# Performance work log

Measured on AMD Instinct MI355X. Metric: run time of the kernel, lower is better.

Reference implementation:

```python
import jax, jax.numpy as jnp
import numpy as np

B, S, D, E, K, FF = 4, 2048, 1024, 8, 2, 4096  # batch, seq, d_model, experts, top-k, 4*d_model


def setup_inputs() -> dict:
    key = jax.random.key(0)
    k0, k1, k2, k3 = jax.random.split(key, 4)
    scale = 0.02
    return {
        "x": jax.random.normal(k0, (B, S, D), jnp.float32),
        "gate_w": jax.random.normal(k1, (D, E), jnp.float32) * scale,
        "w1": jax.random.normal(k2, (E, D, FF), jnp.float32) * scale,
        "b1": jnp.zeros((E, FF), jnp.float32),
        "w2": jax.random.normal(k3, (E, FF, D), jnp.float32) * scale,
        "b2": jnp.zeros((E, D), jnp.float32),
    }


def reference(x, gate_w, w1, b1, w2, b2):
    # Gating: top-k logits, softmax over the selected k (matches torch.topk + softmax)
    logits = jnp.einsum("bsd,de->bse", x, gate_w)  # [B,S,E]
    vals, idxs = jax.lax.top_k(logits, K)           # [B,S,K]
    w = jax.nn.softmax(vals, axis=-1)               # [B,S,K]
    n_exp = gate_w.shape[-1]
    # Per-token combine weight for each expert (0 if not selected)
    combine = jnp.sum(jax.nn.one_hot(idxs, n_exp, dtype=x.dtype) * w[..., None], axis=-2)  # [B,S,E]

    out = jnp.zeros_like(x)
    for e in range(n_exp):  # fixed small loop over experts
        h = jax.nn.silu(jnp.einsum("bsd,df->bsf", x, w1[e]) + b1[e])  # dropout = identity (eval)
        y = jnp.einsum("bsf,fd->bsd", h, w2[e]) + b2[e]
        out = out + combine[..., e:e + 1] * y
    return out
```

## Files before the change

### kernel.cpp

```cpp
#include <hip/hip_runtime.h>
#include <math.h>

#define Tt 8192
#define Dd 1024
#define Ee 8
#define FFf 4096
#define SLOTS (Tt*2)

typedef unsigned short u16;
typedef unsigned int u32;
typedef __attribute__((ext_vector_type(8))) __bf16 bf16x8;
typedef __attribute__((ext_vector_type(4))) float f32x4;

__device__ __forceinline__ u16 f2bf(float f) {
  union { float f; u32 u; } v; v.f = f;
  u32 u = v.u;
  return (u16)((u + 0x7FFFu + ((u >> 16) & 1u)) >> 16);
}
__device__ __forceinline__ float bf2f(u16 h) {
  union { u32 u; float f; } v; v.u = ((u32)h) << 16; return v.f;
}
__device__ __forceinline__ void gl2lds16(const u16* g, u16* l) {
  __builtin_amdgcn_global_load_lds((const __attribute__((address_space(1))) void*)g,
                                   (__attribute__((address_space(3))) void*)l, 16, 0, 0);
}

__global__ void gate_topk_kernel(const float* __restrict__ x,
                                 const float* __restrict__ gw,
                                 int* __restrict__ counts,
                                 int* __restrict__ tok_e,
                                 float* __restrict__ tok_w) {
  int wave = (int)((blockIdx.x * blockDim.x + threadIdx.x) >> 6);
  int lane = threadIdx.x & 63;
  if (wave >= Tt) return;
  const float* xrow = x + (size_t)wave * Dd;
  float p[Ee];
#pragma unroll
  for (int e = 0; e < Ee; e++) p[e] = 0.f;
  int d0 = lane * 16;
#pragma unroll
  for (int i = 0; i < 16; i++) {
    float xv = xrow[d0 + i];
    const float* g = gw + (size_t)(d0 + i) * Ee;
#pragma unroll
    for (int e = 0; e < Ee; e++) p[e] += xv * g[e];
  }
#pragma unroll
  for (int e = 0; e < Ee; e++) {
    for (int off = 32; off > 0; off >>= 1) p[e] += __shfl_xor(p[e], off, 64);
  }
  if (lane == 0) {
    int e0 = 0; float v0 = p[0];
#pragma unroll
    for (int e = 1; e < Ee; e++) if (p[e] > v0) { v0 = p[e]; e0 = e; }
    int e1 = -1; float v1 = -INFINITY;
#pragma unroll
    for (int e = 0; e < Ee; e++) if (e != e0 && p[e] > v1) { v1 = p[e]; e1 = e; }
    float w0 = 1.f / (1.f + expf(v1 - v0));
    float w1 = 1.f - w0;
    tok_e[wave * 2 + 0] = e0; tok_e[wave * 2 + 1] = e1;
    tok_w[wave * 2 + 0] = w0; tok_w[wave * 2 + 1] = w1;
    atomicAdd(&counts[e0], 1);
    atomicAdd(&counts[e1], 1);
  }
}

__global__ void xb_convert_kernel(const float* __restrict__ x, u16* __restrict__ xb) {
  int i = blockIdx.x * blockDim.x + threadIdx.x;
  const float* s = x + (size_t)i * 8;
  f32x4 v0 = *(const f32x4*)(s);
  f32x4 v1 = *(const f32x4*)(s + 4);
  uint4 o;
  o.x = (u32)f2bf(v0[0]) | ((u32)f2bf(v0[1]) << 16);
  o.y = (u32)f2bf(v0[2]) | ((u32)f2bf(v0[3]) << 16);
  o.z = (u32)f2bf(v1[0]) | ((u32)f2bf(v1[1]) << 16);
  o.w = (u32)f2bf(v1[2]) | ((u32)f2bf(v1[3]) << 16);
  *(uint4*)(xb + (size_t)i * 8) = o;
}

__global__ __launch_bounds__(256) void wconv_kernel(const float* __restrict__ src,
                                                    u16* __restrict__ dst, int R, int C) {
  __shared__ u16 t[64][72];
  int e = blockIdx.z;
  size_t ebase = (size_t)e * R * C;
  int r0 = blockIdx.y * 64, c0 = blockIdx.x * 64;
  int tid = threadIdx.x;
  int row = tid >> 2, seg = tid & 3;
  const float* sp = src + ebase + (size_t)(r0 + row) * C + c0 + seg * 16;
  f32x4 v0 = *(const f32x4*)(sp);
  f32x4 v1 = *(const f32x4*)(sp + 4);
  f32x4 v2 = *(const f32x4*)(sp + 8);
  f32x4 v3 = *(const f32x4*)(sp + 12);
  uint4 o0, o1;
  o0.x = (u32)f2bf(v0[0]) | ((u32)f2bf(v0[1]) << 16);
  o0.y = (u32)f2bf(v0[2]) | ((u32)f2bf(v0[3]) << 16);
  o0.z = (u32)f2bf(v1[0]) | ((u32)f2bf(v1[1]) << 16);
  o0.w = (u32)f2bf(v1[2]) | ((u32)f2bf(v1[3]) << 16);
  o1.x = (u32)f2bf(v2[0]) | ((u32)f2bf(v2[1]) << 16);
  o1.y = (u32)f2bf(v2[2]) | ((u32)f2bf(v2[3]) << 16);
  o1.z = (u32)f2bf(v3[0]) | ((u32)f2bf(v3[1]) << 16);
  o1.w = (u32)f2bf(v3[2]) | ((u32)f2bf(v3[3]) << 16);
  *(uint4*)&t[row][seg * 16] = o0;
  *(uint4*)&t[row][seg * 16 + 8] = o1;
  __syncthreads();
  u32 w[8];
#pragma unroll
  for (int i = 0; i < 8; i++)
    w[i] = (u32)t[seg * 16 + 2 * i][row] | ((u32)t[seg * 16 + 2 * i + 1][row] << 16);
  u16* dp = dst + ebase + (size_t)(c0 + row) * R + r0 + seg * 16;
  uint4 d0, d1;
  d0.x = w[0]; d0.y = w[1]; d0.z = w[2]; d0.w = w[3];
  d1.x = w[4]; d1.y = w[5]; d1.z = w[6]; d1.w = w[7];
  *(uint4*)dp = d0;
  *(uint4*)(dp + 8) = d1;
}

__global__ void scan_kernel(const int* __restrict__ counts,
                            int* __restrict__ offsets, int* __restrict__ cursors) {
  if (threadIdx.x == 0 && blockIdx.x == 0) {
    int acc = 0;
    for (int e = 0; e < Ee; e++) { offsets[e] = acc; cursors[e] = acc; acc += counts[e]; }
  }
}

__global__ void scatter_kernel(const int* __restrict__ tok_e, const float* __restrict__ tok_w,
                               int* __restrict__ cursors,
                               int* __restrict__ slot_token, float* __restrict__ slot_w,
                               int* __restrict__ tok_slot) {
  int t = blockIdx.x * blockDim.x + threadIdx.x;
  if (t >= Tt) return;
#pragma unroll
  for (int k = 0; k < 2; k++) {
    int e = tok_e[t * 2 + k];
    int pos = atomicAdd(&cursors[e], 1);
    slot_token[pos] = t;
    slot_w[pos] = tok_w[t * 2 + k];
    tok_slot[t * 2 + k] = pos;
  }
}

#define MFMA16(H)                                                                 \
  do {                                                                            \
    acc[H][0][0] = __builtin_amdgcn_mfma_f32_16x16x32_bf16(a0, b0, acc[H][0][0], 0, 0, 0); \
    acc[H][0][1] = __builtin_amdgcn_mfma_f32_16x16x32_bf16(a0, b1, acc[H][0][1], 0, 0, 0); \
    acc[H][0][2] = __builtin_amdgcn_mfma_f32_16x16x32_bf16(a0, b2, acc[H][0][2], 0, 0, 0); \
    acc[H][0][3] = __builtin_amdgcn_mfma_f32_16x16x32_bf16(a0, b3, acc[H][0][3], 0, 0, 0); \
    acc[H][1][0] = __builtin_amdgcn_mfma_f32_16x16x32_bf16(a1, b0, acc[H][1][0], 0, 0, 0); \
    acc[H][1][1] = __builtin_amdgcn_mfma_f32_16x16x32_bf16(a1, b1, acc[H][1][1], 0, 0, 0); \
    acc[H][1][2] = __builtin_amdgcn_mfma_f32_16x16x32_bf16(a1, b2, acc[H][1][2], 0, 0, 0); \
    acc[H][1][3] = __builtin_amdgcn_mfma_f32_16x16x32_bf16(a1, b3, acc[H][1][3], 0, 0, 0); \
    acc[H][2][0] = __builtin_amdgcn_mfma_f32_16x16x32_bf16(a2, b0, acc[H][2][0], 0, 0, 0); \
    acc[H][2][1] = __builtin_amdgcn_mfma_f32_16x16x32_bf16(a2, b1, acc[H][2][1], 0, 0, 0); \
    acc[H][2][2] = __builtin_amdgcn_mfma_f32_16x16x32_bf16(a2, b2, acc[H][2][2], 0, 0, 0); \
    acc[H][2][3] = __builtin_amdgcn_mfma_f32_16x16x32_bf16(a2, b3, acc[H][2][3], 0, 0, 0); \
    acc[H][3][0] = __builtin_amdgcn_mfma_f32_16x16x32_bf16(a3, b0, acc[H][3][0], 0, 0, 0); \
    acc[H][3][1] = __builtin_amdgcn_mfma_f32_16x16x32_bf16(a3, b1, acc[H][3][1], 0, 0, 0); \
    acc[H][3][2] = __builtin_amdgcn_mfma_f32_16x16x32_bf16(a3, b2, acc[H][3][2], 0, 0, 0); \
    acc[H][3][3] = __builtin_amdgcn_mfma_f32_16x16x32_bf16(a3, b3, acc[H][3][3], 0, 0, 0); \
  } while (0)

template<int KDIM, int NDIM, int EPI, int GATHER>
__global__ __launch_bounds__(512, 2) void moe_gemm_big(
    const u16* __restrict__ A, const u16* __restrict__ BT,
    const float* __restrict__ bias,
    const int* __restrict__ offsets, const int* __restrict__ counts,
    const int* __restrict__ slot_token, const float* __restrict__ slot_w,
    u16* __restrict__ O16, float* __restrict__ Of) {
  constexpr int NT = KDIM / 64;
  int e = blockIdx.z;
  int cnt = counts[e];
  int rb = blockIdx.y;
  if (rb * 256 >= cnt) return;
  int off = offsets[e];
  int n0 = blockIdx.x * 256;

  __shared__ u16 S[65536];

  int tid = threadIdx.x;
  int lane = tid & 63, wave = tid >> 6;
  int wr = wave >> 2, wc = wave & 3;
  int lr = lane & 15, g = lane >> 4;

  const u16* BTe = BT + (size_t)e * NDIM * KDIM;

  const u16* aSrc[2][2];
  const u16* bSrc[2][2];
  int amax = off + cnt - 1;
#pragma unroll
  for (int h = 0; h < 2; h++)
#pragma unroll
    for (int s = 0; s < 2; s++) {
      int c = tid + s * 512;
      int lc = c ^ (((c >> 5) & 1) << 1);
      int ks = lc >> 9, rl = (lc >> 2) & 127, seg = lc & 3;
      int slotRow = off + rb * 256 + h * 128 + rl;
      if (slotRow > amax) slotRow = amax;
      int arow = GATHER ? slot_token[slotRow] : slotRow;
      aSrc[h][s] = A + (size_t)arow * KDIM + ks * 32 + seg * 8;
    }
#pragma unroll
  for (int ks = 0; ks < 2; ks++)
#pragma unroll
    for (int s = 0; s < 2; s++) {
      int c = tid + s * 512;
      int lc = c ^ (((c >> 5) & 1) << 1);
      int row = lc >> 2, seg = lc & 3;
      bSrc[ks][s] = BTe + (size_t)(n0 + row) * KDIM + ks * 32 + seg * 8;
    }

  auto stA = [&](int u, int h) {
    u16* d = &S[(u & 1) * 16384 + h * 8192 + wave * 512];
    gl2lds16(aSrc[h][0] + (size_t)u * 64, d);
    gl2lds16(aSrc[h][1] + (size_t)u * 64, d + 4096);
  };
  auto stB = [&](int u, int ks) {
    u16* d = &S[32768 + (u & 1) * 16384 + ks * 8192 + wave * 512];
    gl2lds16(bSrc[ks][0] + (size_t)u * 64, d);
    gl2lds16(bSrc[ks][1] + (size_t)u * 64, d + 4096);
  };
  auto rdA = [&](int dbuf, int hm, int ks, int i) -> bf16x8 {
    int rl = wr * 64 + i * 16 + lr;
    int logb = ks * 8192 + rl * 64 + g * 16;
    int phys = logb ^ (((rl >> 3) & 1) << 5);
    return *reinterpret_cast<const bf16x8*>(&S[dbuf * 16384 + hm * 8192 + (phys >> 1)]);
  };
  auto rdB = [&](int dbuf, int ks, int j) -> bf16x8 {
    int row = wc * 64 + j * 16 + lr;
    int logb = row * 64 + g * 16;
    int phys = logb ^ (((row >> 3) & 1) << 5);
    return *reinterpret_cast<const bf16x8*>(&S[32768 + dbuf * 16384 + ks * 8192 + (phys >> 1)]);
  };

  f32x4 acc[2][4][4];
#pragma unroll
  for (int h = 0; h < 2; h++)
#pragma unroll
    for (int i = 0; i < 4; i++)
#pragma unroll
      for (int j = 0; j < 4; j++) acc[h][i][j] = (f32x4)(0.0f);

  stB(0, 0); stA(0, 0); stA(0, 1); stB(0, 1);
  stB(1, 0); stA(1, 0);
  asm volatile("s_waitcnt vmcnt(4)" ::: "memory");
  __builtin_amdgcn_s_barrier();

  bf16x8 b0, b1, b2, b3;
  for (int t = 0; t < NT; ++t) {
    int dbuf = t & 1;
    {
      bf16x8 a0 = rdA(dbuf, 0, 0, 0), a1 = rdA(dbuf, 0, 0, 1),
             a2 = rdA(dbuf, 0, 0, 2), a3 = rdA(dbuf, 0, 0, 3);
      b0 = rdB(dbuf, 0, 0); b1 = rdB(dbuf, 0, 1); b2 = rdB(dbuf, 0, 2); b3 = rdB(dbuf, 0, 3);
      if (t + 1 < NT) stA(t + 1, 1);
      __builtin_amdgcn_s_barrier();
      asm volatile("s_waitcnt lgkmcnt(0)" ::: "memory");
      __builtin_amdgcn_sched_barrier(0);
      __builtin_amdgcn_s_setprio(1);
      MFMA16(0);
      __builtin_amdgcn_s_setprio(0);
      __builtin_amdgcn_s_barrier();
    }
    {
      bf16x8 a0 = rdA(dbuf, 1, 0, 0), a1 = rdA(dbuf, 1, 0, 1),
             a2 = rdA(dbuf, 1, 0, 2), a3 = rdA(dbuf, 1, 0, 3);
      if (t + 1 < NT) {
        stB(t + 1, 1);
        asm volatile("s_waitcnt vmcnt(8)" ::: "memory");
      }
      __builtin_amdgcn_s_barrier();
      asm volatile("s_waitcnt lgkmcnt(0)" ::: "memory");
      __builtin_amdgcn_sched_barrier(0);
      __builtin_amdgcn_s_setprio(1);
      MFMA16(1);
      __builtin_amdgcn_s_setprio(0);
      __builtin_amdgcn_s_barrier();
    }
    {
      bf16x8 a0 = rdA(dbuf, 0, 1, 0), a1 = rdA(dbuf, 0, 1, 1),
             a2 = rdA(dbuf, 0, 1, 2), a3 = rdA(dbuf, 0, 1, 3);
      b0 = rdB(dbuf, 1, 0); b1 = rdB(dbuf, 1, 1); b2 = rdB(dbuf, 1, 2); b3 = rdB(dbuf, 1, 3);
      if (t + 2 < NT) stB(t + 2, 0);
      __builtin_amdgcn_s_barrier();
      asm volatile("s_waitcnt lgkmcnt(0)" ::: "memory");
      __builtin_amdgcn_sched_barrier(0);
      __builtin_amdgcn_s_setprio(1);
      MFMA16(0);
      __builtin_amdgcn_s_setprio(0);
      __builtin_amdgcn_s_barrier();
    }
    {
      bf16x8 a0 = rdA(dbuf, 1, 1, 0), a1 = rdA(dbuf, 1, 1, 1),
             a2 = rdA(dbuf, 1, 1, 2), a3 = rdA(dbuf, 1, 1, 3);
      if (t + 2 < NT) {
        stA(t + 2, 0);
        asm volatile("s_waitcnt vmcnt(6)" ::: "memory");
      } else if (t + 1 < NT) {
        asm volatile("s_waitcnt vmcnt(0)" ::: "memory");
      }
      __builtin_amdgcn_s_barrier();
      asm volatile("s_waitcnt lgkmcnt(0)" ::: "memory");
      __builtin_amdgcn_sched_barrier(0);
      __builtin_amdgcn_s_setprio(1);
      MFMA16(1);
      __builtin_amdgcn_s_setprio(0);
      __builtin_amdgcn_s_barrier();
    }
  }

  int rlim = cnt - rb * 256;
#pragma unroll
  for (int hm = 0; hm < 2; hm++)
#pragma unroll
    for (int i = 0; i < 4; i++)
#pragma unroll
      for (int q = 0; q < 4; q++) {
        int m = hm * 128 + wr * 64 + i * 16 + g * 4 + q;
        if (m < rlim) {
          int slot = off + rb * 256 + m;
#pragma unroll
          for (int j = 0; j < 4; j++) {
            int n = n0 + wc * 64 + j * 16 + lr;
            float v = acc[hm][i][j][q] + bias[e * NDIM + n];
            if (EPI == 0) {
              float sv = v / (1.f + expf(-v));
              O16[(size_t)slot * NDIM + n] = f2bf(sv);
            } else if (EPI == 1) {
              O16[(size_t)slot * NDIM + n] = f2bf(v * slot_w[slot]);
            } else {
              atomicAdd(Of + (size_t)slot_token[slot] * NDIM + n, v * slot_w[slot]);
            }
          }
        }
      }
}

template<int KDIM, int NDIM, int EPI, int GATHER>
__global__ __launch_bounds__(256) void moe_gemm_sm(
    const u16* __restrict__ A, const u16* __restrict__ BT,
    const float* __restrict__ bias,
    const int* __restrict__ offsets, const int* __restrict__ counts,
    const int* __restrict__ slot_token, const float* __restrict__ slot_w,
    u16* __restrict__ O16, float* __restrict__ Of) {
  constexpr int NT = KDIM / 64;
  int e = blockIdx.z;
  int cnt = counts[e];
  int rb = blockIdx.y;
  if (rb * 128 >= cnt) return;
  int off = offsets[e];
  int n0 = blockIdx.x * 128;

  __shared__ u16 S[16384];

  int tid = threadIdx.x;
  int lane = tid & 63, wave = tid >> 6;
  int wm = (wave >> 1) * 64, wn = (wave & 1) * 64;
  int lr = lane & 15, g = lane >> 4;

  const u16* BTe = BT + (size_t)e * NDIM * KDIM;
  const u16* aS[4];
  const u16* bS[4];
  int amax = off + cnt - 1;
#pragma unroll
  for (int s = 0; s < 4; s++) {
    int c = tid + s * 256;
    int lc = c ^ (((c >> 5) & 1) << 1);
    int ks = lc >> 9, rl = (lc >> 2) & 127, seg = lc & 3;
    int slotRow = off + rb * 128 + rl;
    if (slotRow > amax) slotRow = amax;
    int arow = GATHER ? slot_token[slotRow] : slotRow;
    aS[s] = A + (size_t)arow * KDIM + ks * 32 + seg * 8;
    bS[s] = BTe + (size_t)(n0 + rl) * KDIM + ks * 32 + seg * 8;
  }

  f32x4 acc[4][4];
#pragma unroll
  for (int i = 0; i < 4; i++)
#pragma unroll
    for (int j = 0; j < 4; j++) acc[i][j] = (f32x4)(0.0f);

  for (int t = 0; t < NT; ++t) {
    __syncthreads();
#pragma unroll
    for (int s = 0; s < 4; s++)
      gl2lds16(aS[s] + (size_t)t * 64, &S[s * 2048 + wave * 512]);
#pragma unroll
    for (int s = 0; s < 4; s++)
      gl2lds16(bS[s] + (size_t)t * 64, &S[8192 + s * 2048 + wave * 512]);
    __syncthreads();
#pragma unroll
    for (int ks = 0; ks < 2; ks++) {
      bf16x8 a[4], b[4];
#pragma unroll
      for (int i = 0; i < 4; i++) {
        int rl = wm + i * 16 + lr;
        int logb = ks * 8192 + rl * 64 + g * 16;
        int phys = logb ^ (((rl >> 3) & 1) << 5);
        a[i] = *reinterpret_cast<const bf16x8*>(&S[phys >> 1]);
      }
#pragma unroll
      for (int j = 0; j < 4; j++) {
        int row = wn + j * 16 + lr;
        int logb = ks * 8192 + row * 64 + g * 16;
        int phys = logb ^ (((row >> 3) & 1) << 5);
        b[j] = *reinterpret_cast<const bf16x8*>(&S[8192 + (phys >> 1)]);
      }
#pragma unroll
      for (int i = 0; i < 4; i++)
#pragma unroll
        for (int j = 0; j < 4; j++)
          acc[i][j] = __builtin_amdgcn_mfma_f32_16x16x32_bf16(a[i], b[j], acc[i][j], 0, 0, 0);
    }
  }

  int rlim = cnt - rb * 128;
#pragma unroll
  for (int i = 0; i < 4; i++)
#pragma unroll
    for (int q = 0; q < 4; q++) {
      int m = wm + i * 16 + g * 4 + q;
      if (m < rlim) {
        int slot = off + rb * 128 + m;
#pragma unroll
        for (int j = 0; j < 4; j++) {
          int n = n0 + wn + j * 16 + lr;
          float v = acc[i][j][q] + bias[e * NDIM + n];
          if (EPI == 0) {
            float sv = v / (1.f + expf(-v));
            O16[(size_t)slot * NDIM + n] = f2bf(sv);
          } else if (EPI == 1) {
            O16[(size_t)slot * NDIM + n] = f2bf(v * slot_w[slot]);
          } else {
            atomicAdd(Of + (size_t)slot_token[slot] * NDIM + n, v * slot_w[slot]);
          }
        }
      }
    }
}

__global__ void combine_kernel(const u16* __restrict__ y, const int* __restrict__ tok_slot,
                               float* __restrict__ out) {
  int gid = blockIdx.x * blockDim.x + threadIdx.x;
  int t = gid >> 7;
  int seg = gid & 127;
  int s0 = tok_slot[t * 2 + 0], s1 = tok_slot[t * 2 + 1];
  uint4 a = *(const uint4*)(y + (size_t)s0 * Dd + seg * 8);
  uint4 b = *(const uint4*)(y + (size_t)s1 * Dd + seg * 8);
  f32x4 o0, o1;
  o0[0] = bf2f((u16)a.x) + bf2f((u16)b.x);
  o0[1] = bf2f((u16)(a.x >> 16)) + bf2f((u16)(b.x >> 16));
  o0[2] = bf2f((u16)a.y) + bf2f((u16)b.y);
  o0[3] = bf2f((u16)(a.y >> 16)) + bf2f((u16)(b.y >> 16));
  o1[0] = bf2f((u16)a.z) + bf2f((u16)b.z);
  o1[1] = bf2f((u16)(a.z >> 16)) + bf2f((u16)(b.z >> 16));
  o1[2] = bf2f((u16)a.w) + bf2f((u16)b.w);
  o1[3] = bf2f((u16)(a.w >> 16)) + bf2f((u16)(b.w >> 16));
  float* op = out + (size_t)t * Dd + seg * 8;
  *(f32x4*)op = o0;
  *(f32x4*)(op + 4) = o1;
}

extern "C" void kernel_launch(void* const* d_in, const int* in_sizes, int n_in,
                              void* d_out, int out_size, void* d_ws, size_t ws_size,
                              hipStream_t stream) {
  const float* x  = (const float*)d_in[0];
  const float* gw = (const float*)d_in[1];
  const float* w1 = (const float*)d_in[2];
  const float* b1 = (const float*)d_in[3];
  const float* w2 = (const float*)d_in[4];
  const float* b2 = (const float*)d_in[5];
  float* out = (float*)d_out;

  char* ws = (char*)d_ws;
  size_t off_counts = 0;
  size_t off_offsets = 256;
  size_t off_cursors = 512;
  size_t off_tok_e = 1024;
  size_t off_tok_w     = off_tok_e + (size_t)Tt * 2 * 4;
  size_t off_tok_slot  = off_tok_w + (size_t)Tt * 2 * 4;
  size_t off_slot_token= off_tok_slot + (size_t)Tt * 2 * 4;
  size_t off_slot_w    = off_slot_token + (size_t)SLOTS * 4;
  size_t off_xb        = off_slot_w + (size_t)SLOTS * 4;
  size_t off_h         = off_xb + (size_t)Tt * Dd * 2;
  size_t off_wT        = off_h + (size_t)SLOTS * FFf * 2;
  size_t off_y         = off_wT + (size_t)Ee * Dd * FFf * 2;
  size_t need_atomic   = off_y;
  size_t need_full     = off_y + (size_t)SLOTS * Dd * 2;
  if (ws_size < need_atomic) return;
  int use_combine = (ws_size >= need_full) ? 1 : 0;

  int* counts     = (int*)(ws + off_counts);
  int* offsets    = (int*)(ws + off_offsets);
  int* cursors    = (int*)(ws + off_cursors);
  int* tok_e      = (int*)(ws + off_tok_e);
  float* tok_w    = (float*)(ws + off_tok_w);
  int* tok_slot   = (int*)(ws + off_tok_slot);
  int* slot_token = (int*)(ws + off_slot_token);
  float* slot_w   = (float*)(ws + off_slot_w);
  u16* xb         = (u16*)(ws + off_xb);
  u16* h          = (u16*)(ws + off_h);
  u16* wT         = (u16*)(ws + off_wT);
  u16* y          = (u16*)(ws + off_y);

  hipMemsetAsync(ws, 0, 1024, stream);

  gate_topk_kernel<<<Tt / 4, 256, 0, stream>>>(x, gw, counts, tok_e, tok_w);
  xb_convert_kernel<<<(Tt * Dd / 8) / 256, 256, 0, stream>>>(x, xb);
  scan_kernel<<<1, 64, 0, stream>>>(counts, offsets, cursors);
  scatter_kernel<<<Tt / 256, 256, 0, stream>>>(tok_e, tok_w, cursors, slot_token, slot_w, tok_slot);

  {
    dim3 gc(FFf / 64, Dd / 64, Ee);
    wconv_kernel<<<gc, 256, 0, stream>>>(w1, wT, Dd, FFf);
  }
  {
    dim3 g1(FFf / 256, Tt / 256, Ee);
    moe_gemm_big<Dd, FFf, 0, 1><<<g1, 512, 0, stream>>>(xb, wT, b1, offsets, counts,
                                                        slot_token, slot_w, h, nullptr);
  }
  {
    dim3 gc(Dd / 64, FFf / 64, Ee);
    wconv_kernel<<<gc, 256, 0, stream>>>(w2, wT, FFf, Dd);
  }
  if (use_combine) {
    dim3 g2(Dd / 128, Tt / 128, Ee);
    moe_gemm_sm<FFf, Dd, 1, 0><<<g2, 256, 0, stream>>>(h, wT, b2, offsets, counts,
                                                       slot_token, slot_w, y, nullptr);
    combine_kernel<<<(Tt * 128) / 256, 256, 0, stream>>>(y, tok_slot, out);
  } else {
    hipMemsetAsync(d_out, 0, (size_t)out_size * sizeof(float), stream);
    dim3 g2(Dd / 128, Tt / 128, Ee);
    moe_gemm_sm<FFf, Dd, 2, 0><<<g2, 256, 0, stream>>>(h, wT, b2, offsets, counts,
                                                       slot_token, slot_w, nullptr, out);
  }
}
```

Measured before the change: 847.0 us.

## Use the 256x256 pipelined GEMM for the second expert GEMM; retune wconv and waitcnt

```diff
diff --git a/kernel.cpp b/kernel.cpp
--- a/kernel.cpp
+++ b/kernel.cpp
@@ -80,37 +80,39 @@
 
 __global__ __launch_bounds__(256) void wconv_kernel(const float* __restrict__ src,
                                                     u16* __restrict__ dst, int R, int C) {
-  __shared__ u16 t[64][72];
+  __shared__ float t[64][65];
   int e = blockIdx.z;
   size_t ebase = (size_t)e * R * C;
   int r0 = blockIdx.y * 64, c0 = blockIdx.x * 64;
   int tid = threadIdx.x;
-  int row = tid >> 2, seg = tid & 3;
-  const float* sp = src + ebase + (size_t)(r0 + row) * C + c0 + seg * 16;
+  int row = tid >> 2, q = tid & 3;
+  const float* sp = src + ebase + (size_t)(r0 + row) * C + c0 + q * 16;
   f32x4 v0 = *(const f32x4*)(sp);
   f32x4 v1 = *(const f32x4*)(sp + 4);
   f32x4 v2 = *(const f32x4*)(sp + 8);
   f32x4 v3 = *(const f32x4*)(sp + 12);
-  uint4 o0, o1;
-  o0.x = (u32)f2bf(v0[0]) | ((u32)f2bf(v0[1]) << 16);
-  o0.y = (u32)f2bf(v0[2]) | ((u32)f2bf(v0[3]) << 16);
-  o0.z = (u32)f2bf(v1[0]) | ((u32)f2bf(v1[1]) << 16);
-  o0.w = (u32)f2bf(v1[2]) | ((u32)f2bf(v1[3]) << 16);
-  o1.x = (u32)f2bf(v2[0]) | ((u32)f2bf(v2[1]) << 16);
-  o1.y = (u32)f2bf(v2[2]) | ((u32)f2bf(v2[3]) << 16);
-  o1.z = (u32)f2bf(v3[0]) | ((u32)f2bf(v3[1]) << 16);
-  o1.w = (u32)f2bf(v3[2]) | ((u32)f2bf(v3[3]) << 16);
-  *(uint4*)&t[row][seg * 16] = o0;
-  *(uint4*)&t[row][seg * 16 + 8] = o1;
+#pragma unroll
+  for (int k = 0; k < 4; k++) t[row][q * 16 + k] = v0[k];
+#pragma unroll
+  for (int k = 0; k < 4; k++) t[row][q * 16 + 4 + k] = v1[k];
+#pragma unroll
+  for (int k = 0; k < 4; k++) t[row][q * 16 + 8 + k] = v2[k];
+#pragma unroll
+  for (int k = 0; k < 4; k++) t[row][q * 16 + 12 + k] = v3[k];
   __syncthreads();
-  u32 w[8];
-#pragma unroll
-  for (int i = 0; i < 8; i++)
-    w[i] = (u32)t[seg * 16 + 2 * i][row] | ((u32)t[seg * 16 + 2 * i + 1][row] << 16);
-  u16* dp = dst + ebase + (size_t)(c0 + row) * R + r0 + seg * 16;
+  float c[16];
+#pragma unroll
+  for (int k = 0; k < 16; k++) c[k] = t[q * 16 + k][row];
   uint4 d0, d1;
-  d0.x = w[0]; d0.y = w[1]; d0.z = w[2]; d0.w = w[3];
-  d1.x = w[4]; d1.y = w[5]; d1.z = w[6]; d1.w = w[7];
+  d0.x = (u32)f2bf(c[0]) | ((u32)f2bf(c[1]) << 16);
+  d0.y = (u32)f2bf(c[2]) | ((u32)f2bf(c[3]) << 16);
+  d0.z = (u32)f2bf(c[4]) | ((u32)f2bf(c[5]) << 16);
+  d0.w = (u32)f2bf(c[6]) | ((u32)f2bf(c[7]) << 16);
+  d1.x = (u32)f2bf(c[8]) | ((u32)f2bf(c[9]) << 16);
+  d1.y = (u32)f2bf(c[10]) | ((u32)f2bf(c[11]) << 16);
+  d1.z = (u32)f2bf(c[12]) | ((u32)f2bf(c[13]) << 16);
+  d1.w = (u32)f2bf(c[14]) | ((u32)f2bf(c[15]) << 16);
+  u16* dp = dst + ebase + (size_t)(c0 + row) * R + r0 + q * 16;
   *(uint4*)dp = d0;
   *(uint4*)(dp + 8) = d1;
 }
@@ -265,7 +267,7 @@
              a2 = rdA(dbuf, 1, 0, 2), a3 = rdA(dbuf, 1, 0, 3);
       if (t + 1 < NT) {
         stB(t + 1, 1);
-        asm volatile("s_waitcnt vmcnt(8)" ::: "memory");
+        asm volatile("s_waitcnt vmcnt(6)" ::: "memory");
       }
       __builtin_amdgcn_s_barrier();
       asm volatile("s_waitcnt lgkmcnt(0)" ::: "memory");
@@ -332,109 +334,6 @@
           }
         }
       }
-}
-
-template<int KDIM, int NDIM, int EPI, int GATHER>
-__global__ __launch_bounds__(256) void moe_gemm_sm(
-    const u16* __restrict__ A, const u16* __restrict__ BT,
-    const float* __restrict__ bias,
-    const int* __restrict__ offsets, const int* __restrict__ counts,
-    const int* __restrict__ slot_token, const float* __restrict__ slot_w,
-    u16* __restrict__ O16, float* __restrict__ Of) {
-  constexpr int NT = KDIM / 64;
-  int e = blockIdx.z;
-  int cnt = counts[e];
-  int rb = blockIdx.y;
-  if (rb * 128 >= cnt) return;
-  int off = offsets[e];
-  int n0 = blockIdx.x * 128;
-
-  __shared__ u16 S[16384];
-
-  int tid = threadIdx.x;
-  int lane = tid & 63, wave = tid >> 6;
-  int wm = (wave >> 1) * 64, wn = (wave & 1) * 64;
-  int lr = lane & 15, g = lane >> 4;
-
-  const u16* BTe = BT + (size_t)e * NDIM * KDIM;
-  const u16* aS[4];
-  const u16* bS[4];
-  int amax = off + cnt - 1;
-#pragma unroll
-  for (int s = 0; s < 4; s++) {
-    int c = tid + s * 256;
-    int lc = c ^ (((c >> 5) & 1) << 1);
-    int ks = lc >> 9, rl = (lc >> 2) & 127, seg = lc & 3;
-    int slotRow = off + rb * 128 + rl;
-    if (slotRow > amax) slotRow = amax;
-    int arow = GATHER ? slot_token[slotRow] : slotRow;
-    aS[s] = A + (size_t)arow * KDIM + ks * 32 + seg * 8;
-    bS[s] = BTe + (size_t)(n0 + rl) * KDIM + ks * 32 + seg * 8;
-  }
-
-  f32x4 acc[4][4];
-#pragma unroll
-  for (int i = 0; i < 4; i++)
-#pragma unroll
-    for (int j = 0; j < 4; j++) acc[i][j] = (f32x4)(0.0f);
-
-  for (int t = 0; t < NT; ++t) {
-    __syncthreads();
-#pragma unroll
-    for (int s = 0; s < 4; s++)
-      gl2lds16(aS[s] + (size_t)t * 64, &S[s * 2048 + wave * 512]);
-#pragma unroll
-    for (int s = 0; s < 4; s++)
-      gl2lds16(bS[s] + (size_t)t * 64, &S[8192 + s * 2048 + wave * 512]);
-    __syncthreads();
-#pragma unroll
-    for (int ks = 0; ks < 2; ks++) {
-      bf16x8 a[4], b[4];
-#pragma unroll
-      for (int i = 0; i < 4; i++) {
-        int rl = wm + i * 16 + lr;
-        int logb = ks * 8192 + rl * 64 + g * 16;
-        int phys = logb ^ (((rl >> 3) & 1) << 5);
-        a[i] = *reinterpret_cast<const bf16x8*>(&S[phys >> 1]);
-      }
-#pragma unroll
-      for (int j = 0; j < 4; j++) {
-        int row = wn + j * 16 + lr;
-        int logb = ks * 8192 + row * 64 + g * 16;
-        int phys = logb ^ (((row >> 3) & 1) << 5);
-        b[j] = *reinterpret_cast<const bf16x8*>(&S[8192 + (phys >> 1)]);
-      }
-#pragma unroll
-      for (int i = 0; i < 4; i++)
-#pragma unroll
-        for (int j = 0; j < 4; j++)
-          acc[i][j] = __builtin_amdgcn_mfma_f32_16x16x32_bf16(a[i], b[j], acc[i][j], 0, 0, 0);
-    }
-  }
-
-  int rlim = cnt - rb * 128;
-#pragma unroll
-  for (int i = 0; i < 4; i++)
-#pragma unroll
-    for (int q = 0; q < 4; q++) {
-      int m = wm + i * 16 + g * 4 + q;
-      if (m < rlim) {
-        int slot = off + rb * 128 + m;
-#pragma unroll
-        for (int j = 0; j < 4; j++) {
-          int n = n0 + wn + j * 16 + lr;
-          float v = acc[i][j][q] + bias[e * NDIM + n];
-          if (EPI == 0) {
-            float sv = v / (1.f + expf(-v));
-            O16[(size_t)slot * NDIM + n] = f2bf(sv);
-          } else if (EPI == 1) {
-            O16[(size_t)slot * NDIM + n] = f2bf(v * slot_w[slot]);
-          } else {
-            atomicAdd(Of + (size_t)slot_token[slot] * NDIM + n, v * slot_w[slot]);
-          }
-        }
-      }
-    }
 }
 
 __global__ void combine_kernel(const u16* __restrict__ y, const int* __restrict__ tok_slot,
@@ -522,14 +421,14 @@
     wconv_kernel<<<gc, 256, 0, stream>>>(w2, wT, FFf, Dd);
   }
   if (use_combine) {
-    dim3 g2(Dd / 128, Tt / 128, Ee);
-    moe_gemm_sm<FFf, Dd, 1, 0><<<g2, 256, 0, stream>>>(h, wT, b2, offsets, counts,
-                                                       slot_token, slot_w, y, nullptr);
+    dim3 g2(Dd / 256, Tt / 256, Ee);
+    moe_gemm_big<FFf, Dd, 1, 0><<<g2, 512, 0, stream>>>(h, wT, b2, offsets, counts,
+                                                        slot_token, slot_w, y, nullptr);
     combine_kernel<<<(Tt * 128) / 256, 256, 0, stream>>>(y, tok_slot, out);
   } else {
     hipMemsetAsync(d_out, 0, (size_t)out_size * sizeof(float), stream);
-    dim3 g2(Dd / 128, Tt / 128, Ee);
-    moe_gemm_sm<FFf, Dd, 2, 0><<<g2, 256, 0, stream>>>(h, wT, b2, offsets, counts,
-                                                       slot_token, slot_w, nullptr, out);
-  }
-}
+    dim3 g2(Dd / 256, Tt / 256, Ee);
+    moe_gemm_big<FFf, Dd, 2, 0><<<g2, 512, 0, stream>>>(h, wT, b2, offsets, counts,
+                                                        slot_token, slot_w, nullptr, out);
+  }
+}
```

Result: faster. 793.2 us (-6.4%).
